# Kernel optimization log

Measured on AMD Instinct MI355X. Metric: run time of the kernel, lower is better.

The kernel has to match this reference:

```python
import jax, jax.numpy as jnp
import numpy as np

N, E, D, H = 50000, 800000, 128, 4

def setup_inputs() -> dict:
    key = jax.random.key(0)
    ks = jax.random.split(key, 6)
    x = jax.random.normal(ks[0], (N, D), dtype=jnp.float32)
    edge_index = jax.random.randint(ks[1], (2, E), 0, N, dtype=jnp.int64)
    W = jax.random.normal(ks[2], (D, H * D), dtype=jnp.float32) * (1.0 / np.sqrt(D))
    att_src = jax.random.normal(ks[3], (H, D), dtype=jnp.float32) * 0.1
    att_dst = jax.random.normal(ks[4], (H, D), dtype=jnp.float32) * 0.1
    bias = jnp.zeros((D,), dtype=jnp.float32)
    gamma = jnp.ones((D,), dtype=jnp.float32)
    beta = jnp.zeros((D,), dtype=jnp.float32)
    return {"x": x, "edge_index": edge_index, "W": W, "att_src": att_src,
            "att_dst": att_dst, "bias": bias, "gamma": gamma, "beta": beta}

def reference(x, edge_index, W, att_src, att_dst, bias, gamma, beta):
    src, dst = edge_index[0], edge_index[1]
    # GATConv: linear transform per head -> [N, H, D]
    xw = (x @ W).reshape(N, H, D)
    a_src = jnp.einsum('nhd,hd->nh', xw, att_src)  # [N, H]
    a_dst = jnp.einsum('nhd,hd->nh', xw, att_dst)  # [N, H]
    alpha = a_src[src] + a_dst[dst]                # [E, H]
    alpha = jax.nn.leaky_relu(alpha, negative_slope=0.2)
    # segment softmax over incoming edges of each dst node
    m = jax.ops.segment_max(alpha, dst, num_segments=N)   # [N, H]
    ex = jnp.exp(alpha - m[dst])                            # [E, H]
    denom = jax.ops.segment_sum(ex, dst, num_segments=N)   # [N, H]
    attn = ex / denom[dst]                                  # [E, H]
    msg = xw[src] * attn[:, :, None]                        # [E, H, D]
    agg = jax.ops.segment_sum(msg, dst, num_segments=N)    # [N, H, D]
    out = agg.mean(axis=1) + bias                           # concat=False: mean heads
    # LayerNorm (eps=1e-5)
    mu = out.mean(axis=-1, keepdims=True)
    var = out.var(axis=-1, keepdims=True)
    out = (out - mu) * jax.lax.rsqrt(var + 1e-5) * gamma + beta
    out = jax.nn.gelu(out, approximate=False)
    return out + x  # project is Identity (in_channels == out_channels)
```

## Files before the change

### kernel.cpp

```cpp
#include <hip/hip_runtime.h>
#include <hip/hip_bf16.h>
#include <hip/hip_fp16.h>
#include <math.h>

#define ND 128
#define NH 4
#define HD 512

typedef __attribute__((ext_vector_type(8))) short bf16x8;
typedef __attribute__((ext_vector_type(4))) float f32x4;

__device__ __forceinline__ unsigned pack_bf16(float a, float b) {
    unsigned ua = __float_as_uint(a), ub = __float_as_uint(b);
    ua = (ua + 0x7fffu + ((ua >> 16) & 1u)) >> 16;
    ub = (ub + 0x7fffu + ((ub >> 16) & 1u)) >> 16;
    return ua | (ub << 16);
}
__device__ __forceinline__ unsigned short bf16r(float a) {
    unsigned ua = __float_as_uint(a);
    return (unsigned short)((ua + 0x7fffu + ((ua >> 16) & 1u)) >> 16);
}
__device__ __forceinline__ float bflo(unsigned u) { return __uint_as_float(u << 16); }
__device__ __forceinline__ float bfhi(unsigned u) { return __uint_as_float(u & 0xffff0000u); }

__device__ __forceinline__ unsigned pack_half2(float a, float b) {
    __half ha = __float2half(a), hb = __float2half(b);
    return (unsigned)__half_as_ushort(ha) | ((unsigned)__half_as_ushort(hb) << 16);
}

__global__ __launch_bounds__(256) void prep_and_hist(const float* __restrict__ W,
                                                     unsigned short* __restrict__ Wt,
                                                     const int* __restrict__ dst,
                                                     int* __restrict__ cnt, int ne) {
    if (blockIdx.x < 256) {
        int idx = blockIdx.x * 256 + threadIdx.x;
        int nl = idx >> 7, k = idx & 127;
        Wt[idx] = bf16r(W[(size_t)k * HD + nl]);
    } else {
        int e = (blockIdx.x - 256) * 256 + threadIdx.x;
        if (e < ne) atomicAdd(&cnt[dst[e]], 1);
    }
}

__global__ __launch_bounds__(256, 2) void gemm_mfma(
        const float* __restrict__ x, const unsigned short* __restrict__ Wt,
        const float* __restrict__ att_src, const float* __restrict__ att_dst,
        unsigned short* __restrict__ xw, float* __restrict__ a_src,
        float* __restrict__ a_dst, int n) {
    __shared__ char lds[65536];
    char* As = lds;
    char* Bs = lds + 32768;
    const int t = threadIdx.x;
    const int row0 = blockIdx.x * 128;
    const int l = t & 63, w = t >> 6;
    const int eid = l & 15, g = l >> 4;

#pragma unroll
    for (int i = 0; i < 8; ++i) {
        int c = t + i * 256;
        int m = c >> 4, kb = c & 15;
        int row = row0 + m;
        uint4 pk;
        if (row < n) {
            const float4* xp = (const float4*)(x + (size_t)row * ND + kb * 8);
            float4 f0 = xp[0], f1 = xp[1];
            pk.x = pack_bf16(f0.x, f0.y); pk.y = pack_bf16(f0.z, f0.w);
            pk.z = pack_bf16(f1.x, f1.y); pk.w = pack_bf16(f1.z, f1.w);
        } else { pk.x = pk.y = pk.z = pk.w = 0u; }
        *(uint4*)(As + m * 256 + ((kb * 16) ^ ((m & 7) << 4))) = pk;
    }

    for (int hh = 0; hh < 2; ++hh) {
        const int h = blockIdx.y * 2 + hh;
        __syncthreads();
#pragma unroll
        for (int i = 0; i < 8; ++i) {
            int c = t + i * 256;
            int nl = c >> 4, kb = c & 15;
            uint4 pv = *(const uint4*)(Wt + (size_t)(h * 128 + nl) * 128 + kb * 8);
            *(uint4*)(Bs + nl * 256 + ((kb * 16) ^ ((nl & 7) << 4))) = pv;
        }
        __syncthreads();

        f32x4 acc[2][8];
#pragma unroll
        for (int mt = 0; mt < 2; ++mt)
#pragma unroll
            for (int nr = 0; nr < 8; ++nr) acc[mt][nr] = (f32x4){0.f, 0.f, 0.f, 0.f};

        const int swz = (eid & 7) << 4;
#pragma unroll
        for (int ks = 0; ks < 4; ++ks) {
            int koff = (ks * 64 + g * 16) ^ swz;
            bf16x8 a0 = *(const bf16x8*)(As + (w * 32 + eid) * 256 + koff);
            bf16x8 a1 = *(const bf16x8*)(As + (w * 32 + 16 + eid) * 256 + koff);
#pragma unroll
            for (int nr = 0; nr < 8; ++nr) {
                bf16x8 b = *(const bf16x8*)(Bs + (nr * 16 + eid) * 256 + koff);
                acc[0][nr] = __builtin_amdgcn_mfma_f32_16x16x32_bf16(a0, b, acc[0][nr], 0, 0, 0);
                acc[1][nr] = __builtin_amdgcn_mfma_f32_16x16x32_bf16(a1, b, acc[1][nr], 0, 0, 0);
            }
        }

        float asv[8], adv[8];
#pragma unroll
        for (int nr = 0; nr < 8; ++nr) {
            asv[nr] = att_src[h * ND + nr * 16 + eid];
            adv[nr] = att_dst[h * ND + nr * 16 + eid];
        }
#pragma unroll
        for (int mt = 0; mt < 2; ++mt) {
#pragma unroll
            for (int ri = 0; ri < 4; ++ri) {
                float s = 0.f, d = 0.f;
#pragma unroll
                for (int nr = 0; nr < 8; ++nr) {
                    s += acc[mt][nr][ri] * asv[nr];
                    d += acc[mt][nr][ri] * adv[nr];
                }
#pragma unroll
                for (int off = 1; off < 16; off <<= 1) {
                    s += __shfl_xor(s, off);
                    d += __shfl_xor(d, off);
                }
                int row = row0 + w * 32 + mt * 16 + g * 4 + ri;
                if (eid == 0 && row < n) {
                    a_src[(size_t)row * NH + h] = s;
                    a_dst[(size_t)row * NH + h] = d;
                }
            }
        }

        __syncthreads();
        unsigned short* Ps = (unsigned short*)Bs;
#pragma unroll
        for (int mt = 0; mt < 2; ++mt)
#pragma unroll
            for (int ri = 0; ri < 4; ++ri) {
                int rl = w * 32 + mt * 16 + g * 4 + ri;
#pragma unroll
                for (int nr = 0; nr < 8; ++nr)
                    Ps[rl * 128 + nr * 16 + eid] = bf16r(acc[mt][nr][ri]);
            }
        __syncthreads();
#pragma unroll
        for (int i = 0; i < 8; ++i) {
            int row = i * 16 + (t >> 4);
            int grow = row0 + row;
            if (grow < n) {
                uint4 v = *(const uint4*)(Ps + row * 128 + (t & 15) * 8);
                *(uint4*)(xw + (size_t)grow * HD + h * ND + (t & 15) * 8) = v;
            }
        }
    }
}

__global__ __launch_bounds__(256) void scanA(const int* __restrict__ cnt,
                                             int* __restrict__ partial,
                                             int* __restrict__ bsum, int n) {
    __shared__ int sh[256];
    int gid = blockIdx.x * 256 + threadIdx.x;
    int v = (gid < n) ? cnt[gid] : 0;
    int val = v;
    sh[threadIdx.x] = val;
    __syncthreads();
#pragma unroll
    for (int off = 1; off < 256; off <<= 1) {
        int add = (threadIdx.x >= off) ? sh[threadIdx.x - off] : 0;
        __syncthreads();
        val += add;
        sh[threadIdx.x] = val;
        __syncthreads();
    }
    if (gid < n) partial[gid] = val - v;
    if (threadIdx.x == 255) bsum[blockIdx.x] = val;
}

__global__ __launch_bounds__(256) void scanBC(const int* __restrict__ partial,
                                              const int* __restrict__ bsum,
                                              int* __restrict__ starts,
                                              int* __restrict__ cursor,
                                              int n, int ne, int nb) {
    __shared__ int sh[256];
    int t = threadIdx.x;
    int v = (t < nb) ? bsum[t] : 0;
    int val = v;
    sh[t] = val;
    __syncthreads();
#pragma unroll
    for (int off = 1; off < 256; off <<= 1) {
        int add = (t >= off) ? sh[t - off] : 0;
        __syncthreads();
        val += add;
        sh[t] = val;
        __syncthreads();
    }
    int myoff = (blockIdx.x == 0) ? 0 : sh[blockIdx.x - 1];
    int gid = blockIdx.x * 256 + t;
    if (gid < n) {
        int s = partial[gid] + myoff;
        starts[gid] = s;
        cursor[gid] = s;
    }
    if (gid == 0) starts[n] = ne;
}

__global__ __launch_bounds__(256) void scatter_edges_w(const int* __restrict__ src,
                                                       const int* __restrict__ dst,
                                                       const float* __restrict__ a_src,
                                                       const float* __restrict__ a_dst,
                                                       int* __restrict__ cursor,
                                                       uint4* __restrict__ eperm, int ne) {
    int e = blockIdx.x * 256 + threadIdx.x;
    if (e < ne) {
        int s = src[e], t = dst[e];
        float4 as = *(const float4*)(a_src + (size_t)s * NH);
        float4 ad = *(const float4*)(a_dst + (size_t)t * NH);
        float A0 = as.x + ad.x, A1 = as.y + ad.y, A2 = as.z + ad.z, A3 = as.w + ad.w;
        A0 = (A0 > 0.f) ? A0 : 0.2f * A0;
        A1 = (A1 > 0.f) ? A1 : 0.2f * A1;
        A2 = (A2 > 0.f) ? A2 : 0.2f * A2;
        A3 = (A3 > 0.f) ? A3 : 0.2f * A3;
        float e0 = expf(A0), e1 = expf(A1), e2 = expf(A2), e3 = expf(A3);
        int pos = atomicAdd(&cursor[t], 1);
        uint4 ev;
        ev.x = (unsigned)s;
        ev.y = pack_half2(e0, e1);
        ev.z = pack_half2(e2, e3);
        ev.w = 0u;
        eperm[pos] = ev;
    }
}

#define ACC4(vv, ww)                                                      \
    acc[0] = fmaf(ww, bflo(vv.x), acc[0]);                                \
    acc[1] = fmaf(ww, bfhi(vv.x), acc[1]);                                \
    acc[2] = fmaf(ww, bflo(vv.y), acc[2]);                                \
    acc[3] = fmaf(ww, bfhi(vv.y), acc[3]);

__global__ __launch_bounds__(256) void node_agg(const uint4* __restrict__ eperm,
                                                const int* __restrict__ starts,
                                                const uint2* __restrict__ xw2,
                                                const float* __restrict__ x,
                                                const float* __restrict__ bias,
                                                const float* __restrict__ gamma,
                                                const float* __restrict__ beta,
                                                float* __restrict__ out, int n) {
    __shared__ float comb[2][32][4];

    const int wib = threadIdx.x >> 6;
    const int lane = threadIdx.x & 63;
    const int pairslot = wib >> 1;
    const int q = wib & 1;
    const int node = blockIdx.x * 2 + pairslot;
    const int hsel = lane >> 5;
    const int slot = lane & 31;
    const int habs = q * 2 + hsel;
    const int hb = hsel << 5;

    const bool alive = (node < n);
    int s0 = 0, s1 = 0;
    if (alive) { s0 = starts[node]; s1 = starts[node + 1]; }

    float den = 0.f;
    float acc[4] = {0.f, 0.f, 0.f, 0.f};

    for (int base = s0; base < s1; base += 32) {
        int rem = s1 - base; if (rem > 32) rem = 32;
        int sl = 0; float em = 0.f;
        if (slot < rem) {
            uint4 ev = eperm[base + slot];
            sl = (int)ev.x;
            unsigned wb2 = (habs & 2) ? ev.z : ev.y;
            unsigned short hbits = (habs & 1) ? (unsigned short)(wb2 >> 16)
                                              : (unsigned short)(wb2 & 0xffffu);
            em = __half2float(__ushort_as_half(hbits));
        }
        den += em;

        int jj = 0;
        for (; jj + 4 <= rem; jj += 4) {
            int t0 = __shfl(sl, jj),     t1 = __shfl(sl, jj + 1);
            int t2 = __shfl(sl, jj + 2), t3 = __shfl(sl, jj + 3);
            uint2 v0 = xw2[(size_t)t0 * 128 + habs * 32 + slot];
            uint2 v1 = xw2[(size_t)t1 * 128 + habs * 32 + slot];
            uint2 v2 = xw2[(size_t)t2 * 128 + habs * 32 + slot];
            uint2 v3 = xw2[(size_t)t3 * 128 + habs * 32 + slot];
            float w0 = __shfl(em, hb + jj);
            float w1 = __shfl(em, hb + jj + 1);
            float w2 = __shfl(em, hb + jj + 2);
            float w3 = __shfl(em, hb + jj + 3);
            ACC4(v0, w0); ACC4(v1, w1); ACC4(v2, w2); ACC4(v3, w3);
        }
        for (; jj < rem; ++jj) {
            int ts = __shfl(sl, jj);
            uint2 v = xw2[(size_t)ts * 128 + habs * 32 + slot];
            float ww = __shfl(em, hb + jj);
            ACC4(v, ww);
        }
    }

#pragma unroll
    for (int off = 1; off < 32; off <<= 1) den += __shfl_xor(den, off);
    float imy = (den > 0.f) ? 0.25f / den : 0.f;

    float v[4];
#pragma unroll
    for (int j = 0; j < 4; ++j) {
        v[j] = acc[j] * imy;
        v[j] += __shfl_xor(v[j], 32);
    }

    if (q == 1 && lane < 32) {
#pragma unroll
        for (int j = 0; j < 4; ++j) comb[pairslot][slot][j] = v[j];
    }
    __syncthreads();
    if (q == 1 || !alive || lane >= 32) return;
#pragma unroll
    for (int j = 0; j < 4; ++j) v[j] += comb[pairslot][slot][j];

    float4 bv = *(const float4*)(bias + slot * 4);
    v[0] += bv.x; v[1] += bv.y; v[2] += bv.z; v[3] += bv.w;

    float s = v[0] + v[1] + v[2] + v[3];
    float s2 = v[0] * v[0] + v[1] * v[1] + v[2] * v[2] + v[3] * v[3];
#pragma unroll
    for (int off = 1; off < 32; off <<= 1) {
        s += __shfl_xor(s, off);
        s2 += __shfl_xor(s2, off);
    }
    float mu = s * (1.0f / ND);
    float var = s2 * (1.0f / ND) - mu * mu;
    var = fmaxf(var, 0.0f);
    float inv = rsqrtf(var + 1e-5f);

    float4 gv = *(const float4*)(gamma + slot * 4);
    float4 tv = *(const float4*)(beta + slot * 4);
    float gm[4] = {gv.x, gv.y, gv.z, gv.w};
    float bt[4] = {tv.x, tv.y, tv.z, tv.w};

    float4 rv = *(const float4*)(x + (size_t)node * ND + slot * 4);
    float rs[4] = {rv.x, rv.y, rv.z, rv.w};

    float y[4];
#pragma unroll
    for (int j = 0; j < 4; ++j) {
        float yn = (v[j] - mu) * inv * gm[j] + bt[j];
        y[j] = 0.5f * yn * (1.0f + erff(yn * 0.70710678118654752f)) + rs[j];
    }
    float4 ov = {y[0], y[1], y[2], y[3]};
    *(float4*)(out + (size_t)node * ND + slot * 4) = ov;
}

extern "C" void kernel_launch(void* const* d_in, const int* in_sizes, int n_in,
                              void* d_out, int out_size, void* d_ws, size_t ws_size,
                              hipStream_t stream) {
    const float* x       = (const float*)d_in[0];
    const int*   edge    = (const int*)d_in[1];
    const float* W       = (const float*)d_in[2];
    const float* att_src = (const float*)d_in[3];
    const float* att_dst = (const float*)d_in[4];
    const float* bias    = (const float*)d_in[5];
    const float* gamma   = (const float*)d_in[6];
    const float* beta    = (const float*)d_in[7];
    float* out = (float*)d_out;

    const int n  = in_sizes[0] / ND;
    const int ne = in_sizes[1] / 2;
    const int* src = edge;
    const int* dst = edge + ne;

    const int nb = (n + 255) / 256;

    char* wsp = (char*)d_ws;
    unsigned short* xw = (unsigned short*)wsp;  wsp += (size_t)n * HD * sizeof(short);
    unsigned short* Wt = (unsigned short*)wsp;  wsp += (size_t)HD * ND * sizeof(short);
    float* a_src   = (float*)wsp;               wsp += (size_t)n * NH * sizeof(float);
    float* a_dst   = (float*)wsp;               wsp += (size_t)n * NH * sizeof(float);
    uint4* eperm   = (uint4*)wsp;               wsp += (size_t)ne * sizeof(uint4);
    int*   cnt     = (int*)wsp;                 wsp += (size_t)n * sizeof(int);
    int*   partial = (int*)wsp;                 wsp += (size_t)n * sizeof(int);
    int*   bsum    = (int*)wsp;                 wsp += 256 * sizeof(int);
    int*   starts  = (int*)wsp;                 wsp += (size_t)(n + 1) * sizeof(int);
    int*   cursor  = (int*)wsp;                 wsp += (size_t)n * sizeof(int);

    hipMemsetAsync(cnt, 0, (size_t)n * sizeof(int), stream);

    prep_and_hist<<<256 + (ne + 255) / 256, 256, 0, stream>>>(W, Wt, dst, cnt, ne);

    dim3 ggrid((n + 127) / 128, 2);
    gemm_mfma<<<ggrid, 256, 0, stream>>>(x, Wt, att_src, att_dst, xw, a_src, a_dst, n);

    scanA<<<nb, 256, 0, stream>>>(cnt, partial, bsum, n);
    scanBC<<<nb, 256, 0, stream>>>(partial, bsum, starts, cursor, n, ne, nb);
    scatter_edges_w<<<(ne + 255) / 256, 256, 0, stream>>>(src, dst, a_src, a_dst,
                                                          cursor, eperm, ne);

    node_agg<<<(n + 1) / 2, 256, 0, stream>>>(
        eperm, starts, (const uint2*)xw, x, bias, gamma, beta, out, n);
}
```

Measured before the change: 239.2 us.

## Aggregate raw bf16 x per head, then apply W after aggregation

Reorders the computation by linearity. Attention logits now come from x dotted with precomputed W·att vectors. Edges are aggregated over 256-byte bf16 x rows instead of 1 KB xw rows, producing per-head weighted sums u of size N×512. A final MFMA GEMM maps u through the stacked W, with LayerNorm, GELU and the residual fused into its epilogue. This cuts gather traffic in node_agg by about four times and removes the xw materialization. In exchange it adds a K=512 GEMM and a bf16 rounding of u.

```diff
diff --git a/kernel.cpp b/kernel.cpp
--- a/kernel.cpp
+++ b/kernel.cpp
@@ -22,135 +22,70 @@
 }
 __device__ __forceinline__ float bflo(unsigned u) { return __uint_as_float(u << 16); }
 __device__ __forceinline__ float bfhi(unsigned u) { return __uint_as_float(u & 0xffff0000u); }
-
 __device__ __forceinline__ unsigned pack_half2(float a, float b) {
     __half ha = __float2half(a), hb = __float2half(b);
     return (unsigned)__half_as_ushort(ha) | ((unsigned)__half_as_ushort(hb) << 16);
 }
-
-__global__ __launch_bounds__(256) void prep_and_hist(const float* __restrict__ W,
-                                                     unsigned short* __restrict__ Wt,
-                                                     const int* __restrict__ dst,
-                                                     int* __restrict__ cnt, int ne) {
-    if (blockIdx.x < 256) {
-        int idx = blockIdx.x * 256 + threadIdx.x;
-        int nl = idx >> 7, k = idx & 127;
-        Wt[idx] = bf16r(W[(size_t)k * HD + nl]);
+__device__ __forceinline__ float2 h22f(unsigned u) {
+    __half2 h = *(__half2*)&u;
+    return __half22float2(h);
+}
+
+__global__ __launch_bounds__(256) void prep_misc(const float* __restrict__ W,
+                                                 const float* __restrict__ att_src,
+                                                 const float* __restrict__ att_dst,
+                                                 unsigned short* __restrict__ Ws,
+                                                 float* __restrict__ pt,
+                                                 const int* __restrict__ dst,
+                                                 int* __restrict__ cnt, int ne) {
+    int b = blockIdx.x;
+    if (b < 256) {
+        int idx = b * 256 + threadIdx.x;
+        int j = idx >> 9, K = idx & 511;
+        int h = K >> 7, k = K & 127;
+        Ws[idx] = bf16r(W[(size_t)k * HD + h * ND + j]);
+    } else if (b == 256) {
+        int k = threadIdx.x;
+        if (k < ND) {
+            for (int h = 0; h < NH; ++h) {
+                float ps = 0.f, pd = 0.f;
+                for (int d = 0; d < ND; ++d) {
+                    float wv = W[(size_t)k * HD + h * ND + d];
+                    ps = fmaf(wv, att_src[h * ND + d], ps);
+                    pd = fmaf(wv, att_dst[h * ND + d], pd);
+                }
+                pt[h * ND + k] = ps;
+                pt[(4 + h) * ND + k] = pd;
+            }
+        }
     } else {
-        int e = (blockIdx.x - 256) * 256 + threadIdx.x;
+        int e = (b - 257) * 256 + threadIdx.x;
         if (e < ne) atomicAdd(&cnt[dst[e]], 1);
     }
 }
 
-__global__ __launch_bounds__(256, 2) void gemm_mfma(
-        const float* __restrict__ x, const unsigned short* __restrict__ Wt,
-        const float* __restrict__ att_src, const float* __restrict__ att_dst,
-        unsigned short* __restrict__ xw, float* __restrict__ a_src,
-        float* __restrict__ a_dst, int n) {
-    __shared__ char lds[65536];
-    char* As = lds;
-    char* Bs = lds + 32768;
-    const int t = threadIdx.x;
-    const int row0 = blockIdx.x * 128;
-    const int l = t & 63, w = t >> 6;
-    const int eid = l & 15, g = l >> 4;
-
-#pragma unroll
-    for (int i = 0; i < 8; ++i) {
-        int c = t + i * 256;
-        int m = c >> 4, kb = c & 15;
-        int row = row0 + m;
-        uint4 pk;
-        if (row < n) {
-            const float4* xp = (const float4*)(x + (size_t)row * ND + kb * 8);
-            float4 f0 = xp[0], f1 = xp[1];
-            pk.x = pack_bf16(f0.x, f0.y); pk.y = pack_bf16(f0.z, f0.w);
-            pk.z = pack_bf16(f1.x, f1.y); pk.w = pack_bf16(f1.z, f1.w);
-        } else { pk.x = pk.y = pk.z = pk.w = 0u; }
-        *(uint4*)(As + m * 256 + ((kb * 16) ^ ((m & 7) << 4))) = pk;
-    }
-
-    for (int hh = 0; hh < 2; ++hh) {
-        const int h = blockIdx.y * 2 + hh;
-        __syncthreads();
-#pragma unroll
-        for (int i = 0; i < 8; ++i) {
-            int c = t + i * 256;
-            int nl = c >> 4, kb = c & 15;
-            uint4 pv = *(const uint4*)(Wt + (size_t)(h * 128 + nl) * 128 + kb * 8);
-            *(uint4*)(Bs + nl * 256 + ((kb * 16) ^ ((nl & 7) << 4))) = pv;
-        }
-        __syncthreads();
-
-        f32x4 acc[2][8];
-#pragma unroll
-        for (int mt = 0; mt < 2; ++mt)
-#pragma unroll
-            for (int nr = 0; nr < 8; ++nr) acc[mt][nr] = (f32x4){0.f, 0.f, 0.f, 0.f};
-
-        const int swz = (eid & 7) << 4;
-#pragma unroll
-        for (int ks = 0; ks < 4; ++ks) {
-            int koff = (ks * 64 + g * 16) ^ swz;
-            bf16x8 a0 = *(const bf16x8*)(As + (w * 32 + eid) * 256 + koff);
-            bf16x8 a1 = *(const bf16x8*)(As + (w * 32 + 16 + eid) * 256 + koff);
-#pragma unroll
-            for (int nr = 0; nr < 8; ++nr) {
-                bf16x8 b = *(const bf16x8*)(Bs + (nr * 16 + eid) * 256 + koff);
-                acc[0][nr] = __builtin_amdgcn_mfma_f32_16x16x32_bf16(a0, b, acc[0][nr], 0, 0, 0);
-                acc[1][nr] = __builtin_amdgcn_mfma_f32_16x16x32_bf16(a1, b, acc[1][nr], 0, 0, 0);
-            }
-        }
-
-        float asv[8], adv[8];
-#pragma unroll
-        for (int nr = 0; nr < 8; ++nr) {
-            asv[nr] = att_src[h * ND + nr * 16 + eid];
-            adv[nr] = att_dst[h * ND + nr * 16 + eid];
-        }
-#pragma unroll
-        for (int mt = 0; mt < 2; ++mt) {
-#pragma unroll
-            for (int ri = 0; ri < 4; ++ri) {
-                float s = 0.f, d = 0.f;
-#pragma unroll
-                for (int nr = 0; nr < 8; ++nr) {
-                    s += acc[mt][nr][ri] * asv[nr];
-                    d += acc[mt][nr][ri] * adv[nr];
-                }
-#pragma unroll
-                for (int off = 1; off < 16; off <<= 1) {
-                    s += __shfl_xor(s, off);
-                    d += __shfl_xor(d, off);
-                }
-                int row = row0 + w * 32 + mt * 16 + g * 4 + ri;
-                if (eid == 0 && row < n) {
-                    a_src[(size_t)row * NH + h] = s;
-                    a_dst[(size_t)row * NH + h] = d;
-                }
-            }
-        }
-
-        __syncthreads();
-        unsigned short* Ps = (unsigned short*)Bs;
-#pragma unroll
-        for (int mt = 0; mt < 2; ++mt)
-#pragma unroll
-            for (int ri = 0; ri < 4; ++ri) {
-                int rl = w * 32 + mt * 16 + g * 4 + ri;
-#pragma unroll
-                for (int nr = 0; nr < 8; ++nr)
-                    Ps[rl * 128 + nr * 16 + eid] = bf16r(acc[mt][nr][ri]);
-            }
-        __syncthreads();
-#pragma unroll
-        for (int i = 0; i < 8; ++i) {
-            int row = i * 16 + (t >> 4);
-            int grow = row0 + row;
-            if (grow < n) {
-                uint4 v = *(const uint4*)(Ps + row * 128 + (t & 15) * 8);
-                *(uint4*)(xw + (size_t)grow * HD + h * ND + (t & 15) * 8) = v;
-            }
+__global__ __launch_bounds__(256) void k_a_xb(const float* __restrict__ x,
+                                              const float* __restrict__ pt,
+                                              unsigned* __restrict__ xb,
+                                              float* __restrict__ a_src,
+                                              float* __restrict__ a_dst, int n) {
+    __shared__ float pl[8 * ND];
+    { int t = threadIdx.x; ((float4*)pl)[t] = ((const float4*)pt)[t]; }
+    __syncthreads();
+    int wave = (blockIdx.x * 256 + threadIdx.x) >> 6;
+    int lane = threadIdx.x & 63;
+    if (wave >= n) return;
+    float2 xv = ((const float2*)(x + (size_t)wave * ND))[lane];
+    xb[(size_t)wave * 64 + lane] = pack_bf16(xv.x, xv.y);
+#pragma unroll
+    for (int o = 0; o < 8; ++o) {
+        float2 pv = ((const float2*)(pl + o * ND))[lane];
+        float v = xv.x * pv.x + xv.y * pv.y;
+#pragma unroll
+        for (int off = 1; off < 64; off <<= 1) v += __shfl_xor(v, off);
+        if (lane == 0) {
+            if (o < 4) a_src[(size_t)wave * NH + o] = v;
+            else       a_dst[(size_t)wave * NH + (o - 4)] = v;
         }
     }
 }
@@ -232,125 +167,197 @@
     }
 }
 
-#define ACC4(vv, ww)                                                      \
-    acc[0] = fmaf(ww, bflo(vv.x), acc[0]);                                \
-    acc[1] = fmaf(ww, bfhi(vv.x), acc[1]);                                \
-    acc[2] = fmaf(ww, bflo(vv.y), acc[2]);                                \
-    acc[3] = fmaf(ww, bfhi(vv.y), acc[3]);
+#define FMA16()                                                            \
+    { float f0 = bflo(xv.x), f1 = bfhi(xv.x), f2 = bflo(xv.y), f3 = bfhi(xv.y); \
+      acc[0] = fmaf(w01.x, f0, acc[0]);  acc[1] = fmaf(w01.x, f1, acc[1]);  \
+      acc[2] = fmaf(w01.x, f2, acc[2]);  acc[3] = fmaf(w01.x, f3, acc[3]);  \
+      acc[4] = fmaf(w01.y, f0, acc[4]);  acc[5] = fmaf(w01.y, f1, acc[5]);  \
+      acc[6] = fmaf(w01.y, f2, acc[6]);  acc[7] = fmaf(w01.y, f3, acc[7]);  \
+      acc[8] = fmaf(w23.x, f0, acc[8]);  acc[9] = fmaf(w23.x, f1, acc[9]);  \
+      acc[10] = fmaf(w23.x, f2, acc[10]); acc[11] = fmaf(w23.x, f3, acc[11]); \
+      acc[12] = fmaf(w23.y, f0, acc[12]); acc[13] = fmaf(w23.y, f1, acc[13]); \
+      acc[14] = fmaf(w23.y, f2, acc[14]); acc[15] = fmaf(w23.y, f3, acc[15]); }
 
 __global__ __launch_bounds__(256) void node_agg(const uint4* __restrict__ eperm,
                                                 const int* __restrict__ starts,
-                                                const uint2* __restrict__ xw2,
-                                                const float* __restrict__ x,
-                                                const float* __restrict__ bias,
-                                                const float* __restrict__ gamma,
-                                                const float* __restrict__ beta,
-                                                float* __restrict__ out, int n) {
-    __shared__ float comb[2][32][4];
-
-    const int wib = threadIdx.x >> 6;
-    const int lane = threadIdx.x & 63;
-    const int pairslot = wib >> 1;
-    const int q = wib & 1;
-    const int node = blockIdx.x * 2 + pairslot;
-    const int hsel = lane >> 5;
+                                                const uint2* __restrict__ xb2,
+                                                unsigned* __restrict__ u, int n) {
+    int node = (blockIdx.x * 256 + threadIdx.x) >> 6;
+    int lane = threadIdx.x & 63;
+    if (node >= n) return;
     const int slot = lane & 31;
-    const int habs = q * 2 + hsel;
-    const int hb = hsel << 5;
-
-    const bool alive = (node < n);
-    int s0 = 0, s1 = 0;
-    if (alive) { s0 = starts[node]; s1 = starts[node + 1]; }
-
-    float den = 0.f;
-    float acc[4] = {0.f, 0.f, 0.f, 0.f};
-
-    for (int base = s0; base < s1; base += 32) {
-        int rem = s1 - base; if (rem > 32) rem = 32;
-        int sl = 0; float em = 0.f;
-        if (slot < rem) {
-            uint4 ev = eperm[base + slot];
-            sl = (int)ev.x;
-            unsigned wb2 = (habs & 2) ? ev.z : ev.y;
-            unsigned short hbits = (habs & 1) ? (unsigned short)(wb2 >> 16)
-                                              : (unsigned short)(wb2 & 0xffffu);
-            em = __half2float(__ushort_as_half(hbits));
-        }
-        den += em;
-
-        int jj = 0;
-        for (; jj + 4 <= rem; jj += 4) {
-            int t0 = __shfl(sl, jj),     t1 = __shfl(sl, jj + 1);
-            int t2 = __shfl(sl, jj + 2), t3 = __shfl(sl, jj + 3);
-            uint2 v0 = xw2[(size_t)t0 * 128 + habs * 32 + slot];
-            uint2 v1 = xw2[(size_t)t1 * 128 + habs * 32 + slot];
-            uint2 v2 = xw2[(size_t)t2 * 128 + habs * 32 + slot];
-            uint2 v3 = xw2[(size_t)t3 * 128 + habs * 32 + slot];
-            float w0 = __shfl(em, hb + jj);
-            float w1 = __shfl(em, hb + jj + 1);
-            float w2 = __shfl(em, hb + jj + 2);
-            float w3 = __shfl(em, hb + jj + 3);
-            ACC4(v0, w0); ACC4(v1, w1); ACC4(v2, w2); ACC4(v3, w3);
-        }
-        for (; jj < rem; ++jj) {
-            int ts = __shfl(sl, jj);
-            uint2 v = xw2[(size_t)ts * 128 + habs * 32 + slot];
-            float ww = __shfl(em, hb + jj);
-            ACC4(v, ww);
-        }
-    }
-
-#pragma unroll
-    for (int off = 1; off < 32; off <<= 1) den += __shfl_xor(den, off);
-    float imy = (den > 0.f) ? 0.25f / den : 0.f;
-
-    float v[4];
-#pragma unroll
-    for (int j = 0; j < 4; ++j) {
-        v[j] = acc[j] * imy;
-        v[j] += __shfl_xor(v[j], 32);
-    }
-
-    if (q == 1 && lane < 32) {
-#pragma unroll
-        for (int j = 0; j < 4; ++j) comb[pairslot][slot][j] = v[j];
-    }
+    const int half = lane >> 5;
+
+    int s0 = starts[node], s1 = starts[node + 1];
+
+    float den0 = 0.f, den1 = 0.f, den2 = 0.f, den3 = 0.f;
+    float acc[16];
+#pragma unroll
+    for (int j = 0; j < 16; ++j) acc[j] = 0.f;
+
+    for (int base = s0; base < s1; base += 16) {
+        int rem = s1 - base; if (rem > 16) rem = 16;
+        uint4 ev = {0u, 0u, 0u, 0u};
+        if (lane < rem) ev = eperm[base + lane];
+        {
+            float2 dl = h22f(ev.y), dh = h22f(ev.z);
+            den0 += dl.x; den1 += dl.y; den2 += dh.x; den3 += dh.y;
+        }
+        if (rem == 16) {
+#pragma unroll
+            for (int pp = 0; pp < 8; ++pp) {
+                int j2 = 2 * pp + half;
+                int s = __shfl((int)ev.x, j2);
+                unsigned uy = __shfl(ev.y, j2);
+                unsigned uz = __shfl(ev.z, j2);
+                uint2 xv = xb2[(size_t)s * 32 + slot];
+                float2 w01 = h22f(uy), w23 = h22f(uz);
+                FMA16();
+            }
+        } else {
+            for (int jj = 0; jj < rem; jj += 2) {
+                int j2 = jj + half;
+                bool valid = (j2 < rem);
+                int j2c = valid ? j2 : jj;
+                int s = __shfl((int)ev.x, j2c);
+                unsigned uy = __shfl(ev.y, j2c);
+                unsigned uz = __shfl(ev.z, j2c);
+                uint2 xv = xb2[(size_t)s * 32 + slot];
+                float2 w01 = h22f(uy), w23 = h22f(uz);
+                float m = valid ? 1.f : 0.f;
+                w01.x *= m; w01.y *= m; w23.x *= m; w23.y *= m;
+                FMA16();
+            }
+        }
+    }
+
+#pragma unroll
+    for (int off = 1; off < 64; off <<= 1) {
+        den0 += __shfl_xor(den0, off);
+        den1 += __shfl_xor(den1, off);
+        den2 += __shfl_xor(den2, off);
+        den3 += __shfl_xor(den3, off);
+    }
+    float i0 = (den0 > 0.f) ? 0.25f / den0 : 0.f;
+    float i1 = (den1 > 0.f) ? 0.25f / den1 : 0.f;
+    float i2 = (den2 > 0.f) ? 0.25f / den2 : 0.f;
+    float i3 = (den3 > 0.f) ? 0.25f / den3 : 0.f;
+
+    float v[16];
+#pragma unroll
+    for (int f = 0; f < 4; ++f) {
+        v[0 + f]  = acc[0 + f]  * i0;
+        v[4 + f]  = acc[4 + f]  * i1;
+        v[8 + f]  = acc[8 + f]  * i2;
+        v[12 + f] = acc[12 + f] * i3;
+    }
+#pragma unroll
+    for (int j = 0; j < 16; ++j) v[j] += __shfl_xor(v[j], 32);
+
+#pragma unroll
+    for (int hh = 0; hh < 2; ++hh) {
+        int h = half * 2 + hh;
+        uint2 val;
+        val.x = pack_bf16(v[h * 4 + 0], v[h * 4 + 1]);
+        val.y = pack_bf16(v[h * 4 + 2], v[h * 4 + 3]);
+        ((uint2*)u)[(size_t)node * 128 + h * 32 + slot] = val;
+    }
+}
+
+__global__ __launch_bounds__(256, 2) void gemm_out(
+        const unsigned short* __restrict__ u, const unsigned short* __restrict__ Ws,
+        const float* __restrict__ x, const float* __restrict__ bias,
+        const float* __restrict__ gamma, const float* __restrict__ beta,
+        float* __restrict__ out, int n) {
+    __shared__ char lds[65536];
+    char* As = lds;
+    char* Bs = lds + 32768;
+    const int t = threadIdx.x;
+    const int row0 = blockIdx.x * 128;
+    const int l = t & 63, w = t >> 6;
+    const int eid = l & 15, g = l >> 4;
+
+    f32x4 acc[2][8];
+#pragma unroll
+    for (int mt = 0; mt < 2; ++mt)
+#pragma unroll
+        for (int nr = 0; nr < 8; ++nr) acc[mt][nr] = (f32x4){0.f, 0.f, 0.f, 0.f};
+
+    for (int kc = 0; kc < 4; ++kc) {
+        __syncthreads();
+#pragma unroll
+        for (int i = 0; i < 8; ++i) {
+            int c = t + i * 256;
+            int m = c >> 4, kb = c & 15;
+            int row = row0 + m;
+            uint4 pv = {0u, 0u, 0u, 0u};
+            if (row < n) pv = *(const uint4*)(u + (size_t)row * HD + kc * 128 + kb * 8);
+            *(uint4*)(As + m * 256 + ((kb * 16) ^ ((m & 7) << 4))) = pv;
+        }
+#pragma unroll
+        for (int i = 0; i < 8; ++i) {
+            int c = t + i * 256;
+            int nl = c >> 4, kb = c & 15;
+            uint4 pv = *(const uint4*)(Ws + (size_t)nl * HD + kc * 128 + kb * 8);
+            *(uint4*)(Bs + nl * 256 + ((kb * 16) ^ ((nl & 7) << 4))) = pv;
+        }
+        __syncthreads();
+
+        const int swz = (eid & 7) << 4;
+#pragma unroll
+        for (int ks = 0; ks < 4; ++ks) {
+            int koff = (ks * 64 + g * 16) ^ swz;
+            bf16x8 a0 = *(const bf16x8*)(As + (w * 32 + eid) * 256 + koff);
+            bf16x8 a1 = *(const bf16x8*)(As + (w * 32 + 16 + eid) * 256 + koff);
+#pragma unroll
+            for (int nr = 0; nr < 8; ++nr) {
+                bf16x8 b = *(const bf16x8*)(Bs + (nr * 16 + eid) * 256 + koff);
+                acc[0][nr] = __builtin_amdgcn_mfma_f32_16x16x32_bf16(a0, b, acc[0][nr], 0, 0, 0);
+                acc[1][nr] = __builtin_amdgcn_mfma_f32_16x16x32_bf16(a1, b, acc[1][nr], 0, 0, 0);
+            }
+        }
+    }
+
     __syncthreads();
-    if (q == 1 || !alive || lane >= 32) return;
-#pragma unroll
-    for (int j = 0; j < 4; ++j) v[j] += comb[pairslot][slot][j];
-
-    float4 bv = *(const float4*)(bias + slot * 4);
-    v[0] += bv.x; v[1] += bv.y; v[2] += bv.z; v[3] += bv.w;
-
-    float s = v[0] + v[1] + v[2] + v[3];
-    float s2 = v[0] * v[0] + v[1] * v[1] + v[2] * v[2] + v[3] * v[3];
-#pragma unroll
-    for (int off = 1; off < 32; off <<= 1) {
-        s += __shfl_xor(s, off);
-        s2 += __shfl_xor(s2, off);
-    }
-    float mu = s * (1.0f / ND);
-    float var = s2 * (1.0f / ND) - mu * mu;
-    var = fmaxf(var, 0.0f);
-    float inv = rsqrtf(var + 1e-5f);
-
-    float4 gv = *(const float4*)(gamma + slot * 4);
-    float4 tv = *(const float4*)(beta + slot * 4);
-    float gm[4] = {gv.x, gv.y, gv.z, gv.w};
-    float bt[4] = {tv.x, tv.y, tv.z, tv.w};
-
-    float4 rv = *(const float4*)(x + (size_t)node * ND + slot * 4);
-    float rs[4] = {rv.x, rv.y, rv.z, rv.w};
-
-    float y[4];
-#pragma unroll
-    for (int j = 0; j < 4; ++j) {
-        float yn = (v[j] - mu) * inv * gm[j] + bt[j];
-        y[j] = 0.5f * yn * (1.0f + erff(yn * 0.70710678118654752f)) + rs[j];
-    }
-    float4 ov = {y[0], y[1], y[2], y[3]};
-    *(float4*)(out + (size_t)node * ND + slot * 4) = ov;
+    float* T = (float*)lds;
+#pragma unroll
+    for (int mt = 0; mt < 2; ++mt)
+#pragma unroll
+        for (int ri = 0; ri < 4; ++ri) {
+            int rl = w * 32 + mt * 16 + g * 4 + ri;
+#pragma unroll
+            for (int nr = 0; nr < 8; ++nr)
+                T[rl * 128 + nr * 16 + eid] = acc[mt][nr][ri];
+        }
+    __syncthreads();
+
+    float2 bv = ((const float2*)bias)[l];
+    float2 gv = ((const float2*)gamma)[l];
+    float2 tb = ((const float2*)beta)[l];
+    for (int i = 0; i < 32; ++i) {
+        int row = w * 32 + i;
+        int grow = row0 + row;
+        if (grow >= n) break;
+        float2 c2 = ((float2*)(T + row * 128))[l];
+        c2.x += bv.x; c2.y += bv.y;
+        float s = c2.x + c2.y, s2 = c2.x * c2.x + c2.y * c2.y;
+#pragma unroll
+        for (int off = 1; off < 64; off <<= 1) {
+            s += __shfl_xor(s, off);
+            s2 += __shfl_xor(s2, off);
+        }
+        float mu = s * (1.0f / ND);
+        float var = s2 * (1.0f / ND) - mu * mu;
+        var = fmaxf(var, 0.0f);
+        float inv = rsqrtf(var + 1e-5f);
+        float2 xres = ((const float2*)(x + (size_t)grow * ND))[l];
+        float y0 = (c2.x - mu) * inv * gv.x + tb.x;
+        float y1 = (c2.y - mu) * inv * gv.y + tb.y;
+        y0 = 0.5f * y0 * (1.0f + erff(y0 * 0.70710678118654752f)) + xres.x;
+        y1 = 0.5f * y1 * (1.0f + erff(y1 * 0.70710678118654752f)) + xres.y;
+        float2 ov = {y0, y1};
+        ((float2*)(out + (size_t)grow * ND))[l] = ov;
+    }
 }
 
 extern "C" void kernel_launch(void* const* d_in, const int* in_sizes, int n_in,
@@ -374,8 +381,10 @@
     const int nb = (n + 255) / 256;
 
     char* wsp = (char*)d_ws;
-    unsigned short* xw = (unsigned short*)wsp;  wsp += (size_t)n * HD * sizeof(short);
-    unsigned short* Wt = (unsigned short*)wsp;  wsp += (size_t)HD * ND * sizeof(short);
+    unsigned* xb        = (unsigned*)wsp;        wsp += (size_t)n * 64 * sizeof(unsigned);
+    unsigned short* u   = (unsigned short*)wsp;  wsp += (size_t)n * HD * sizeof(short);
+    unsigned short* Ws  = (unsigned short*)wsp;  wsp += (size_t)ND * HD * sizeof(short);
+    float* pt      = (float*)wsp;               wsp += (size_t)8 * ND * sizeof(float);
     float* a_src   = (float*)wsp;               wsp += (size_t)n * NH * sizeof(float);
     float* a_dst   = (float*)wsp;               wsp += (size_t)n * NH * sizeof(float);
     uint4* eperm   = (uint4*)wsp;               wsp += (size_t)ne * sizeof(uint4);
@@ -385,18 +394,19 @@
     int*   starts  = (int*)wsp;                 wsp += (size_t)(n + 1) * sizeof(int);
     int*   cursor  = (int*)wsp;                 wsp += (size_t)n * sizeof(int);
 
-    hipMemsetAsync(cnt, 0, (size_t)n * sizeof(int), stream);
-
-    prep_and_hist<<<256 + (ne + 255) / 256, 256, 0, stream>>>(W, Wt, dst, cnt, ne);
-
-    dim3 ggrid((n + 127) / 128, 2);
-    gemm_mfma<<<ggrid, 256, 0, stream>>>(x, Wt, att_src, att_dst, xw, a_src, a_dst, n);
+    (void)hipMemsetAsync(cnt, 0, (size_t)n * sizeof(int), stream);
+
+    prep_misc<<<257 + (ne + 255) / 256, 256, 0, stream>>>(W, att_src, att_dst,
+                                                          Ws, pt, dst, cnt, ne);
+    k_a_xb<<<(n + 3) / 4, 256, 0, stream>>>(x, pt, xb, a_src, a_dst, n);
 
     scanA<<<nb, 256, 0, stream>>>(cnt, partial, bsum, n);
     scanBC<<<nb, 256, 0, stream>>>(partial, bsum, starts, cursor, n, ne, nb);
     scatter_edges_w<<<(ne + 255) / 256, 256, 0, stream>>>(src, dst, a_src, a_dst,
                                                           cursor, eperm, ne);
 
-    node_agg<<<(n + 1) / 2, 256, 0, stream>>>(
-        eperm, starts, (const uint2*)xw, x, bias, gamma, beta, out, n);
-}
+    node_agg<<<(n + 3) / 4, 256, 0, stream>>>(eperm, starts, (const uint2*)xb,
+                                              (unsigned*)u, n);
+
+    gemm_out<<<(n + 127) / 128, 256, 0, stream>>>(u, Ws, x, bias, gamma, beta, out, n);
+}
```

Result: slower. 246.5 us (+3.1%).
